# Kernel optimization log

Hardware: AMD Instinct MI355X
Metric: run time of the kernel (lower is better)

## Reference

```python
import jax, jax.numpy as jnp
import numpy as np

V, D, L, H, F, K, T_MAX = 50265, 768, 12, 12, 3072, 2, 512
DH = D // H
EPS = 1e-12


def _ln(x, w, b):
    mu = jnp.mean(x, axis=-1, keepdims=True)
    var = jnp.mean(jnp.square(x - mu), axis=-1, keepdims=True)
    return (x - mu) * jax.lax.rsqrt(var + EPS) * w + b


def setup_inputs() -> dict:
    key = jax.random.key(0)
    ks = iter(jax.random.split(key, 32))
    B, T = 8, 512
    inp = {}
    inp['input_ids'] = jax.random.randint(next(ks), (B, T), 0, V, dtype=jnp.int64)
    inp['attention_mask'] = jnp.ones((B, T), dtype=jnp.int32)
    s = 0.02
    inp['tok_emb'] = jax.random.normal(next(ks), (V, D), jnp.float32) * s
    inp['pos_emb'] = jax.random.normal(next(ks), (T_MAX, D), jnp.float32) * s
    inp['lang_emb'] = jax.random.normal(next(ks), (K, D), jnp.float32) * s
    inp['switch_emb'] = jax.random.normal(next(ks), (D,), jnp.float32) * s
    # prototypes: orthogonal-ish rows scaled by 0.5
    P = jax.random.normal(next(ks), (K, D), jnp.float32)
    Pq, _ = jnp.linalg.qr(P.T)  # (D, K) orthonormal cols
    inp['prototypes'] = Pq.T * 0.5
    inp['log_tau'] = jnp.array(0.0, jnp.float32)  # log(1.0)
    inp['emb_ln_w'] = jnp.ones((D,), jnp.float32)
    inp['emb_ln_b'] = jnp.zeros((D,), jnp.float32)
    # per-layer params, stacked with leading L dim; Linear weights stored torch-style (out,in)
    inp['Wq'] = jax.random.normal(next(ks), (L, D, D), jnp.float32) * s
    inp['Wk'] = jax.random.normal(next(ks), (L, D, D), jnp.float32) * s
    inp['Wv'] = jax.random.normal(next(ks), (L, D, D), jnp.float32) * s
    inp['Wo'] = jax.random.normal(next(ks), (L, D, D), jnp.float32) * s
    inp['Wo_b'] = jnp.zeros((L, D), jnp.float32)
    inp['compat'] = jnp.broadcast_to(jnp.eye(K), (L, H, K, K)) + 0.01 * jax.random.normal(next(ks), (L, H, K, K), jnp.float32)
    inp['gamma'] = jnp.zeros((L,), jnp.float32)
    inp['W1'] = jax.random.normal(next(ks), (L, F, D), jnp.float32) * s
    inp['b1'] = jnp.zeros((L, F), jnp.float32)
    inp['W2'] = jax.random.normal(next(ks), (L, D, F), jnp.float32) * s
    inp['b2'] = jnp.zeros((L, D), jnp.float32)
    inp['ln1_w'] = jnp.ones((L, D), jnp.float32)
    inp['ln1_b'] = jnp.zeros((L, D), jnp.float32)
    inp['ln2_w'] = jnp.ones((L, D), jnp.float32)
    inp['ln2_b'] = jnp.zeros((L, D), jnp.float32)
    return inp


def reference(input_ids, attention_mask, tok_emb, pos_emb, lang_emb, switch_emb,
              prototypes, log_tau, emb_ln_w, emb_ln_b,
              Wq, Wk, Wv, Wo, Wo_b, compat, gamma,
              W1, b1, W2, b2, ln1_w, ln1_b, ln2_w, ln2_b):
    B, T = input_ids.shape
    # Stage 1: raw base embedding (tok + pos)
    h_base = tok_emb[input_ids] + pos_emb[jnp.arange(T)][None, :, :]  # (B,T,D)
    # pre-contextual language distributions p0 and switch magnitudes s
    tau = jnp.maximum(jnp.exp(log_tau), 0.25)
    p = jax.nn.softmax(jnp.einsum('btd,kd->btk', h_base, prototypes) / tau, axis=-1)  # (B,T,K)
    sim = jnp.sum(p[:, 1:] * p[:, :-1], axis=-1)
    s = jnp.concatenate([jnp.zeros((B, 1), p.dtype), 1.0 - sim], axis=1)  # (B,T)
    # Stage 2: augment + LN (dropout is identity in eval)
    h = _ln(h_base + p @ lang_emb + s[..., None] * switch_emb, emb_ln_w, emb_ln_b)
    additive = (1.0 - attention_mask.astype(h.dtype))[:, None, None, :] * -10000.0  # (B,1,1,T)
    scale = 1.0 / np.sqrt(DH)
    for l in range(L):
        q = jnp.einsum('btd,ed->bte', h, Wq[l]).reshape(B, T, H, DH).transpose(0, 2, 1, 3)
        k = jnp.einsum('btd,ed->bte', h, Wk[l]).reshape(B, T, H, DH).transpose(0, 2, 1, 3)
        v = jnp.einsum('btd,ed->bte', h, Wv[l]).reshape(B, T, H, DH).transpose(0, 2, 1, 3)
        scores = jnp.einsum('bhid,bhjd->bhij', q, k) * scale
        # per-head language compatibility bias p_i^T C_h p_j
        p_compat = jnp.einsum('bik,hkl->bhil', p, compat[l])
        scores = scores + jnp.einsum('bhil,bjl->bhij', p_compat, p)
        scores = scores + gamma[l] * s[:, None, None, :]
        scores = scores + additive
        attn = jax.nn.softmax(scores, axis=-1)
        ctx = jnp.einsum('bhij,bhjd->bhid', attn, v).transpose(0, 2, 1, 3).reshape(B, T, D)
        attn_out = jnp.einsum('btd,ed->bte', ctx, Wo[l]) + Wo_b[l]
        h_mid = _ln(h + attn_out, ln1_w[l], ln1_b[l])
        ffn = jnp.einsum('btf,df->btd', jax.nn.gelu(jnp.einsum('btd,fd->btf', h_mid, W1[l]) + b1[l], approximate=False), W2[l]) + b2[l]
        h = _ln(h_mid + ffn, ln2_w[l], ln2_b[l])
    return h
```

## Files before the change

kernel.cpp:

```cpp
#include <hip/hip_runtime.h>
#include <hip/hip_bf16.h>
#include <math.h>


typedef __bf16 bf16;
typedef __attribute__((ext_vector_type(8))) __bf16 bf16x8;
typedef __attribute__((ext_vector_type(4))) __bf16 bf16x4;
typedef __attribute__((ext_vector_type(4))) float f32x4;

#define N_TOK 4096
#define D_SZ 768
#define F_SZ 3072
#define L_SZ 12
#define MN_SZ ((size_t)N_TOK * D_SZ)
#define SPITCH 516
#define PPITCH 520

__device__ __forceinline__ void async_ld16(const void* g, void* l) {
  __builtin_amdgcn_global_load_lds((const __attribute__((address_space(1))) void*)g,
                                   (__attribute__((address_space(3))) void*)l, 16, 0, 0);
}

__device__ inline void block_reduce2(float& a, float& b, int tid) {
  #pragma unroll
  for (int off = 32; off; off >>= 1) {
    a += __shfl_xor(a, off);
    b += __shfl_xor(b, off);
  }
  __shared__ float red[8];
  if ((tid & 63) == 0) { red[tid >> 6] = a; red[4 + (tid >> 6)] = b; }
  __syncthreads();
  a = red[0] + red[1] + red[2] + red[3];
  b = red[4] + red[5] + red[6] + red[7];
  __syncthreads();
}

__global__ void __launch_bounds__(256) f2b_kernel(const float* __restrict__ src,
                                                  bf16* __restrict__ dst, int n4) {
  int i = blockIdx.x * 256 + threadIdx.x;
  if (i >= n4) return;
  float4 v = ((const float4*)src)[i];
  bf16x4 o; o.x = (bf16)v.x; o.y = (bf16)v.y; o.z = (bf16)v.z; o.w = (bf16)v.w;
  *(bf16x4*)(dst + (size_t)i * 4) = o;
}

__global__ void __launch_bounds__(256) build_wqkv_kernel(const float* __restrict__ Wq,
    const float* __restrict__ Wk, const float* __restrict__ Wv, bf16* __restrict__ dst) {
  int i = blockIdx.x * 256 + threadIdx.x;
  const int per_layer = 2304 * 768;
  long idx = (long)i * 4;
  if (idx >= 12L * per_layer) return;
  int l = (int)(idx / per_layer);
  int rem = (int)(idx - (long)l * per_layer);
  int r = rem / 768;
  int c = rem - r * 768;
  const float* src;
  if (r < 768)       src = Wq + ((size_t)l * 768 + r) * 768 + c;
  else if (r < 1536) src = Wk + ((size_t)l * 768 + (r - 768)) * 768 + c;
  else               src = Wv + ((size_t)l * 768 + (r - 1536)) * 768 + c;
  float4 v = *(const float4*)src;
  bf16x4 o; o.x = (bf16)v.x; o.y = (bf16)v.y; o.z = (bf16)v.z; o.w = (bf16)v.w;
  *(bf16x4*)(dst + idx) = o;
}

__global__ void __launch_bounds__(256) embed_a_kernel(const int* __restrict__ ids,
    const float* __restrict__ tok, const float* __restrict__ pos,
    const float* __restrict__ proto, const float* __restrict__ log_tau,
    float* __restrict__ h_base, float* __restrict__ p_out) {
  int n = blockIdx.x;
  int t = n & 511;
  int tid = threadIdx.x;
  int id = ids[n];
  float d0 = 0.f, d1 = 0.f;
  #pragma unroll
  for (int jj = 0; jj < 3; jj++) {
    int j = tid + jj * 256;
    float v = tok[(size_t)id * 768 + j] + pos[(size_t)t * 768 + j];
    h_base[(size_t)n * 768 + j] = v;
    d0 += v * proto[j];
    d1 += v * proto[768 + j];
  }
  block_reduce2(d0, d1, tid);
  if (tid == 0) {
    float tau = fmaxf(__expf(log_tau[0]), 0.25f);
    float a = d0 / tau, bb = d1 / tau;
    float m = fmaxf(a, bb);
    float e0 = __expf(a - m), e1 = __expf(bb - m);
    float si = e0 + e1;
    p_out[n * 2] = e0 / si;
    p_out[n * 2 + 1] = e1 / si;
  }
}

__global__ void __launch_bounds__(256) embed_c_kernel(const float* __restrict__ h_base,
    const float* __restrict__ p, const float* __restrict__ lang, const float* __restrict__ sw,
    const float* __restrict__ lw, const float* __restrict__ lb,
    float* __restrict__ s_out, float* __restrict__ h_out, bf16* __restrict__ h_bf) {
  int n = blockIdx.x;
  int t = n & 511;
  int tid = threadIdx.x;
  float p0 = p[n * 2], p1 = p[n * 2 + 1];
  float sv = 0.f;
  if (t > 0) sv = 1.f - (p0 * p[(n - 1) * 2] + p1 * p[(n - 1) * 2 + 1]);
  if (tid == 0) s_out[n] = sv;
  float x[3]; float sum = 0.f, sq = 0.f;
  #pragma unroll
  for (int jj = 0; jj < 3; jj++) {
    int j = tid + jj * 256;
    float v = h_base[(size_t)n * 768 + j] + p0 * lang[j] + p1 * lang[768 + j] + sv * sw[j];
    x[jj] = v; sum += v; sq += v * v;
  }
  block_reduce2(sum, sq, tid);
  float mean = sum * (1.f / 768.f);
  float var = fmaxf(sq * (1.f / 768.f) - mean * mean, 0.f);
  float inv = rsqrtf(var + 1e-12f);
  #pragma unroll
  for (int jj = 0; jj < 3; jj++) {
    int j = tid + jj * 256;
    float o = (x[jj] - mean) * inv * lw[j] + lb[j];
    h_out[(size_t)n * 768 + j] = o;
    h_bf[(size_t)n * 768 + j] = (bf16)o;
  }
}

template <int NZ>
__global__ void __launch_bounds__(256) ln5_kernel(const float* __restrict__ x1,
    const float* __restrict__ t, const float* __restrict__ bias,
    const float* __restrict__ w, const float* __restrict__ bv,
    float* __restrict__ out_f, bf16* __restrict__ out_b) {
  int n = blockIdx.x;
  int tid = threadIdx.x;
  float x[3]; float sum = 0.f, sq = 0.f;
  #pragma unroll
  for (int jj = 0; jj < 3; jj++) {
    int j = tid + jj * 256;
    size_t o = (size_t)n * 768 + j;
    float v = x1[o] + bias[j];
    #pragma unroll
    for (int z = 0; z < NZ; z++) v += t[o + (size_t)z * MN_SZ];
    x[jj] = v; sum += v; sq += v * v;
  }
  block_reduce2(sum, sq, tid);
  float mean = sum * (1.f / 768.f);
  float var = fmaxf(sq * (1.f / 768.f) - mean * mean, 0.f);
  float inv = rsqrtf(var + 1e-12f);
  #pragma unroll
  for (int jj = 0; jj < 3; jj++) {
    int j = tid + jj * 256;
    float o = (x[jj] - mean) * inv * w[j] + bv[j];
    out_f[(size_t)n * 768 + j] = o;
    out_b[(size_t)n * 768 + j] = (bf16)o;
  }
}

template <int MODE>
__global__ void __launch_bounds__(256) gemm_nt(const bf16* __restrict__ A,
    const bf16* __restrict__ B, void* __restrict__ C, bf16* __restrict__ C2,
    const float* __restrict__ bias, int M, int N, int K) {
  __shared__ bf16 As[128 * 32];
  __shared__ bf16 Bs[128 * 32];
  const int tid = threadIdx.x;
  const int lane = tid & 63;
  const int wave = tid >> 6;
  const int wm = wave >> 1, wn = wave & 1;
  const int m0 = blockIdx.x * 128, n0 = blockIdx.y * 128;
  const int fr = lane & 15, fq = lane >> 4;
  const int srow = wave * 16 + (lane >> 2);
  const int scol = (lane & 3) * 8;

  int kb = 0, ke = K;
  if (MODE == 1) { int ks = K / gridDim.z; kb = blockIdx.z * ks; ke = kb + ks; }

  f32x4 acc[4][4] = {};
  const bf16* Ap = A + (size_t)(m0 + srow) * K + scol;
  const bf16* Bp = B + (size_t)(n0 + srow) * K + scol;
  bf16* AsW = &As[wave * 512];
  bf16* BsW = &Bs[wave * 512];
  for (int k0 = kb; k0 < ke; k0 += 32) {
    async_ld16(Ap + k0, AsW);
    async_ld16(Ap + (size_t)64 * K + k0, AsW + 64 * 32);
    async_ld16(Bp + k0, BsW);
    async_ld16(Bp + (size_t)64 * K + k0, BsW + 64 * 32);
    __syncthreads();
    bf16x8 af[4], bfr[4];
    #pragma unroll
    for (int i = 0; i < 4; i++) af[i]  = *(const bf16x8*)&As[(wm * 64 + i * 16 + fr) * 32 + fq * 8];
    #pragma unroll
    for (int i = 0; i < 4; i++) bfr[i] = *(const bf16x8*)&Bs[(wn * 64 + i * 16 + fr) * 32 + fq * 8];
    #pragma unroll
    for (int i = 0; i < 4; i++)
      #pragma unroll
      for (int j = 0; j < 4; j++)
        acc[i][j] = __builtin_amdgcn_mfma_f32_16x16x32_bf16(af[i], bfr[j], acc[i][j], 0, 0, 0);
    __syncthreads();
  }

  const bool vregion = (MODE == 3) && (n0 >= 1536);
  float* Cz = (MODE == 1) ? ((float*)C + (size_t)blockIdx.z * M * N) : (float*)C;
  #pragma unroll
  for (int i = 0; i < 4; i++) {
    int row0 = m0 + wm * 64 + i * 16 + fq * 4;
    #pragma unroll
    for (int j = 0; j < 4; j++) {
      int col = n0 + wn * 64 + j * 16 + fr;
      if (MODE == 3 && vregion) {
        int vcol = col - 1536;
        int h = vcol >> 6, dh = vcol & 63;
        int b = row0 >> 9, t0 = row0 & 511;
        bf16x4 o;
        #pragma unroll
        for (int r = 0; r < 4; r++) o[r] = (bf16)acc[i][j][r];
        *(bf16x4*)&C2[((size_t)(b * 12 + h) * 64 + dh) * 512 + t0] = o;
      } else {
        #pragma unroll
        for (int r = 0; r < 4; r++) {
          float v = acc[i][j][r];
          if (MODE == 2) {
            v += bias[col];
            v = 0.5f * v * (1.f + erff(v * 0.70710678118654752f));
          }
          if (MODE == 1)      Cz[(size_t)(row0 + r) * N + col] = v;
          else if (MODE == 3) ((bf16*)C)[(size_t)(row0 + r) * 1536 + col] = (bf16)v;
          else                ((bf16*)C)[(size_t)(row0 + r) * N + col] = (bf16)v;
        }
      }
    }
  }
}

__global__ void __launch_bounds__(256) attn_kernel(const bf16* __restrict__ qkv,
    const bf16* __restrict__ vt, const float* __restrict__ p, const float* __restrict__ s,
    const int* __restrict__ mask, const float* __restrict__ compat,
    const float* __restrict__ gamma, int l, bf16* __restrict__ ctx) {
  __shared__ float scb[32 * SPITCH];
  const int tid = threadIdx.x;
  const int lane = tid & 63;
  const int w = tid >> 6;
  const int fr = lane & 15, fq = lane >> 4;
  const int qc = blockIdx.x, h = blockIdx.y, b = blockIdx.z;
  const int i0 = qc * 32;
  const float* Cm = compat + (size_t)(l * 12 + h) * 4;
  const float gl = gamma[l];

  bf16x8 qf[2][2];
  #pragma unroll
  for (int mt = 0; mt < 2; mt++)
    #pragma unroll
    for (int kk = 0; kk < 2; kk++)
      qf[mt][kk] = *(const bf16x8*)&qkv[(size_t)(b * 512 + i0 + mt * 16 + fr) * 1536 + h * 64 + kk * 32 + fq * 8];
  for (int ntl = 0; ntl < 8; ++ntl) {
    int j0 = (w * 8 + ntl) * 16;
    bf16x8 kf0 = *(const bf16x8*)&qkv[(size_t)(b * 512 + j0 + fr) * 1536 + 768 + h * 64 + fq * 8];
    bf16x8 kf1 = *(const bf16x8*)&qkv[(size_t)(b * 512 + j0 + fr) * 1536 + 768 + h * 64 + 32 + fq * 8];
    #pragma unroll
    for (int mt = 0; mt < 2; mt++) {
      f32x4 acc = {};
      acc = __builtin_amdgcn_mfma_f32_16x16x32_bf16(qf[mt][0], kf0, acc, 0, 0, 0);
      acc = __builtin_amdgcn_mfma_f32_16x16x32_bf16(qf[mt][1], kf1, acc, 0, 0, 0);
      #pragma unroll
      for (int r = 0; r < 4; r++)
        scb[(mt * 16 + fq * 4 + r) * SPITCH + j0 + fr] = acc[r] * 0.125f;
    }
  }

  float pj0[8], pj1[8], basej[8];
  #pragma unroll
  for (int jj = 0; jj < 8; jj++) {
    int j = lane + jj * 64;
    pj0[jj] = p[(b * 512 + j) * 2];
    pj1[jj] = p[(b * 512 + j) * 2 + 1];
    basej[jj] = gl * s[b * 512 + j] + (1.f - (float)mask[b * 512 + j]) * -10000.f;
  }
  __syncthreads();

  float xs[8][8];
  #pragma unroll
  for (int il = 0; il < 8; ++il) {
    int i = w * 8 + il;
    int qi = i0 + i;
    float p0 = p[(b * 512 + qi) * 2], p1 = p[(b * 512 + qi) * 2 + 1];
    float cp0 = p0 * Cm[0] + p1 * Cm[2];
    float cp1 = p0 * Cm[1] + p1 * Cm[3];
    float mx = -3.0e38f;
    #pragma unroll
    for (int jj = 0; jj < 8; jj++) {
      float v = scb[i * SPITCH + lane + jj * 64] + cp0 * pj0[jj] + cp1 * pj1[jj] + basej[jj];
      xs[il][jj] = v; mx = fmaxf(mx, v);
    }
    #pragma unroll
    for (int off = 32; off; off >>= 1) mx = fmaxf(mx, __shfl_xor(mx, off));
    float sum = 0.f;
    #pragma unroll
    for (int jj = 0; jj < 8; jj++) { float e = __expf(xs[il][jj] - mx); xs[il][jj] = e; sum += e; }
    #pragma unroll
    for (int off = 32; off; off >>= 1) sum += __shfl_xor(sum, off);
    float inv = 1.f / sum;
    #pragma unroll
    for (int jj = 0; jj < 8; jj++) xs[il][jj] *= inv;
  }
  __syncthreads();

  bf16* pbf = (bf16*)scb;
  #pragma unroll
  for (int il = 0; il < 8; ++il)
    #pragma unroll
    for (int jj = 0; jj < 8; jj++)
      pbf[(w * 8 + il) * PPITCH + lane + jj * 64] = (bf16)xs[il][jj];
  __syncthreads();

  const int mt3 = w & 1;
  const int ntb = (w >> 1) * 2;
  f32x4 acc3[2] = {};
  for (int kt = 0; kt < 16; ++kt) {
    bf16x8 af = *(const bf16x8*)&pbf[(mt3 * 16 + fr) * PPITCH + kt * 32 + fq * 8];
    #pragma unroll
    for (int np = 0; np < 2; np++) {
      bf16x8 vf = *(const bf16x8*)&vt[(size_t)((b * 12 + h) * 64 + (ntb + np) * 16 + fr) * 512 + kt * 32 + fq * 8];
      acc3[np] = __builtin_amdgcn_mfma_f32_16x16x32_bf16(af, vf, acc3[np], 0, 0, 0);
    }
  }
  #pragma unroll
  for (int np = 0; np < 2; np++)
    #pragma unroll
    for (int r = 0; r < 4; r++)
      ctx[(size_t)(b * 512 + i0 + mt3 * 16 + fq * 4 + r) * 768 + h * 64 + (ntb + np) * 16 + fr] = (bf16)acc3[np][r];
}

extern "C" void kernel_launch(void* const* d_in, const int* in_sizes, int n_in,
                              void* d_out, int out_size, void* d_ws, size_t ws_size,
                              hipStream_t stream) {
  const int*   input_ids  = (const int*)d_in[0];
  const int*   attn_mask  = (const int*)d_in[1];
  const float* tok_emb    = (const float*)d_in[2];
  const float* pos_emb    = (const float*)d_in[3];
  const float* lang_emb   = (const float*)d_in[4];
  const float* switch_emb = (const float*)d_in[5];
  const float* prototypes = (const float*)d_in[6];
  const float* log_tau    = (const float*)d_in[7];
  const float* emb_ln_w   = (const float*)d_in[8];
  const float* emb_ln_b   = (const float*)d_in[9];
  const float* Wq   = (const float*)d_in[10];
  const float* Wk   = (const float*)d_in[11];
  const float* Wv   = (const float*)d_in[12];
  const float* Wo   = (const float*)d_in[13];
  const float* Wo_b = (const float*)d_in[14];
  const float* compat = (const float*)d_in[15];
  const float* gamma  = (const float*)d_in[16];
  const float* W1   = (const float*)d_in[17];
  const float* b1   = (const float*)d_in[18];
  const float* W2   = (const float*)d_in[19];
  const float* b2   = (const float*)d_in[20];
  const float* ln1_w = (const float*)d_in[21];
  const float* ln1_b = (const float*)d_in[22];
  const float* ln2_w = (const float*)d_in[23];
  const float* ln2_b = (const float*)d_in[24];

  char* wsp = (char*)d_ws;
  size_t off = 0;
  auto alloc = [&](size_t bytes) { void* pp = wsp + off; off += (bytes + 255) & ~(size_t)255; return pp; };
  float* h_f      = (float*)alloc(MN_SZ * 4);
  bf16*  h_bf     = (bf16*)alloc(MN_SZ * 2);
  float* h_mid    = (float*)alloc(MN_SZ * 4);
  bf16*  h_mid_bf = (bf16*)alloc(MN_SZ * 2);
  float* tmp      = (float*)alloc(MN_SZ * 4 * 4);
  float* h_base   = tmp + 3 * MN_SZ;
  float* p_buf    = (float*)alloc((size_t)N_TOK * 2 * 4);
  float* s_buf    = (float*)alloc((size_t)N_TOK * 4);
  bf16*  qkv      = (bf16*)alloc((size_t)N_TOK * 1536 * 2);
  bf16*  vt       = (bf16*)alloc(MN_SZ * 2);
  bf16*  ctx      = (bf16*)alloc(MN_SZ * 2);
  bf16*  a1       = (bf16*)alloc((size_t)N_TOK * F_SZ * 2);
  bf16*  wqkv_bf  = (bf16*)alloc((size_t)L_SZ * 2304 * 768 * 2);
  bf16*  wo_bf    = (bf16*)alloc((size_t)L_SZ * 768 * 768 * 2);
  bf16*  w1_bf    = (bf16*)alloc((size_t)L_SZ * 3072 * 768 * 2);
  bf16*  w2_bf    = (bf16*)alloc((size_t)L_SZ * 768 * 3072 * 2);
  (void)ws_size; (void)in_sizes; (void)n_in; (void)out_size;

  build_wqkv_kernel<<<(12 * 2304 * 768 / 4 + 255) / 256, 256, 0, stream>>>(Wq, Wk, Wv, wqkv_bf);
  f2b_kernel<<<(12 * 768 * 768 / 4 + 255) / 256, 256, 0, stream>>>(Wo, wo_bf, 12 * 768 * 768 / 4);
  f2b_kernel<<<(12 * 3072 * 768 / 4 + 255) / 256, 256, 0, stream>>>(W1, w1_bf, 12 * 3072 * 768 / 4);
  f2b_kernel<<<(12 * 768 * 3072 / 4 + 255) / 256, 256, 0, stream>>>(W2, w2_bf, 12 * 768 * 3072 / 4);

  embed_a_kernel<<<N_TOK, 256, 0, stream>>>(input_ids, tok_emb, pos_emb, prototypes, log_tau,
                                            h_base, p_buf);
  embed_c_kernel<<<N_TOK, 256, 0, stream>>>(h_base, p_buf, lang_emb, switch_emb, emb_ln_w,
                                            emb_ln_b, s_buf, h_f, h_bf);

  for (int l = 0; l < 12; ++l) {
    gemm_nt<3><<<dim3(32, 18), 256, 0, stream>>>(h_bf, wqkv_bf + (size_t)l * 2304 * 768, qkv,
                                                 vt, nullptr, N_TOK, 2304, 768);
    attn_kernel<<<dim3(16, 12, 8), 256, 0, stream>>>(qkv, vt, p_buf, s_buf, attn_mask,
                                                     compat, gamma, l, ctx);
    gemm_nt<1><<<dim3(32, 6, 2), 256, 0, stream>>>(ctx, wo_bf + (size_t)l * 768 * 768, tmp,
                                                   nullptr, nullptr, N_TOK, 768, 768);
    ln5_kernel<2><<<N_TOK, 256, 0, stream>>>(h_f, tmp, Wo_b + l * 768,
                                             ln1_w + l * 768, ln1_b + l * 768, h_mid, h_mid_bf);
    gemm_nt<2><<<dim3(32, 24), 256, 0, stream>>>(h_mid_bf, w1_bf + (size_t)l * 3072 * 768, a1,
                                                 nullptr, b1 + l * 3072, N_TOK, 3072, 768);
    gemm_nt<1><<<dim3(32, 6, 4), 256, 0, stream>>>(a1, w2_bf + (size_t)l * 768 * 3072, tmp,
                                                   nullptr, nullptr, N_TOK, 768, 3072);
    float* hdst = (l == 11) ? (float*)d_out : h_f;
    ln5_kernel<4><<<N_TOK, 256, 0, stream>>>(h_mid, tmp, b2 + l * 768,
                                             ln2_w + l * 768, ln2_b + l * 768, hdst, h_bf);
  }
}
```

Measured before the change: 2.838 ms.

## Widen GEMM K-tile to 64 with XOR-swizzled LDS layout

Doubles the K depth of each shared-memory tile in the bf16 MFMA GEMM from 32 to 64, which halves the number of barrier pairs per output tile. The LDS layout also gains an XOR swizzle on 16-byte chunks, so that fragment reads by the 16 rows of a wave avoid bank conflicts. Doubling the shared-memory footprint may lower occupancy. The async global-to-LDS loads are rearranged so each wave fills 8-row stripes.

```diff
diff --git a/kernel.cpp b/kernel.cpp
--- a/kernel.cpp
+++ b/kernel.cpp
@@ -157,41 +157,50 @@
 __global__ void __launch_bounds__(256) gemm_nt(const bf16* __restrict__ A,
     const bf16* __restrict__ B, void* __restrict__ C, bf16* __restrict__ C2,
     const float* __restrict__ bias, int M, int N, int K) {
-  __shared__ bf16 As[128 * 32];
-  __shared__ bf16 Bs[128 * 32];
+  __shared__ __align__(16) bf16 As[128 * 64];
+  __shared__ __align__(16) bf16 Bs[128 * 64];
   const int tid = threadIdx.x;
   const int lane = tid & 63;
   const int wave = tid >> 6;
   const int wm = wave >> 1, wn = wave & 1;
   const int m0 = blockIdx.x * 128, n0 = blockIdx.y * 128;
   const int fr = lane & 15, fq = lane >> 4;
-  const int srow = wave * 16 + (lane >> 2);
-  const int scol = (lane & 3) * 8;
+  const int lrow = lane >> 3;
+  const int lcol = ((lane & 7) ^ lrow) << 3;
+  const int xsw = (fr & 7) << 4;
 
   int kb = 0, ke = K;
   if (MODE == 1) { int ks = K / gridDim.z; kb = blockIdx.z * ks; ke = kb + ks; }
 
   f32x4 acc[4][4] = {};
-  const bf16* Ap = A + (size_t)(m0 + srow) * K + scol;
-  const bf16* Bp = B + (size_t)(n0 + srow) * K + scol;
-  bf16* AsW = &As[wave * 512];
-  bf16* BsW = &Bs[wave * 512];
-  for (int k0 = kb; k0 < ke; k0 += 32) {
-    async_ld16(Ap + k0, AsW);
-    async_ld16(Ap + (size_t)64 * K + k0, AsW + 64 * 32);
-    async_ld16(Bp + k0, BsW);
-    async_ld16(Bp + (size_t)64 * K + k0, BsW + 64 * 32);
+  const bf16* Ap = A + (size_t)(m0 + wave * 8 + lrow) * K + lcol;
+  const bf16* Bp = B + (size_t)(n0 + wave * 8 + lrow) * K + lcol;
+  bf16* AsW = &As[wave * 8 * 64];
+  bf16* BsW = &Bs[wave * 8 * 64];
+  for (int k0 = kb; k0 < ke; k0 += 64) {
+    #pragma unroll
+    for (int c = 0; c < 4; c++) {
+      async_ld16(Ap + (size_t)(c * 32) * K + k0, AsW + c * 32 * 64);
+      async_ld16(Bp + (size_t)(c * 32) * K + k0, BsW + c * 32 * 64);
+    }
     __syncthreads();
-    bf16x8 af[4], bfr[4];
-    #pragma unroll
-    for (int i = 0; i < 4; i++) af[i]  = *(const bf16x8*)&As[(wm * 64 + i * 16 + fr) * 32 + fq * 8];
-    #pragma unroll
-    for (int i = 0; i < 4; i++) bfr[i] = *(const bf16x8*)&Bs[(wn * 64 + i * 16 + fr) * 32 + fq * 8];
-    #pragma unroll
-    for (int i = 0; i < 4; i++)
+    #pragma unroll
+    for (int kk = 0; kk < 2; kk++) {
+      bf16x8 af[4], bfr[4];
       #pragma unroll
-      for (int j = 0; j < 4; j++)
-        acc[i][j] = __builtin_amdgcn_mfma_f32_16x16x32_bf16(af[i], bfr[j], acc[i][j], 0, 0, 0);
+      for (int i = 0; i < 4; i++)
+        af[i] = *(const bf16x8*)((const char*)As +
+                 (wm * 64 + i * 16 + fr) * 128 + ((kk * 64 + fq * 16) ^ xsw));
+      #pragma unroll
+      for (int i = 0; i < 4; i++)
+        bfr[i] = *(const bf16x8*)((const char*)Bs +
+                 (wn * 64 + i * 16 + fr) * 128 + ((kk * 64 + fq * 16) ^ xsw));
+      #pragma unroll
+      for (int i = 0; i < 4; i++)
+        #pragma unroll
+        for (int j = 0; j < 4; j++)
+          acc[i][j] = __builtin_amdgcn_mfma_f32_16x16x32_bf16(af[i], bfr[j], acc[i][j], 0, 0, 0);
+    }
     __syncthreads();
   }
 
```

Measured after the change: 2.799 ms. No clear change (-1.4%).
